# Kernel optimization log

Hardware: AMD Instinct MI355X
Metric: run time of the kernel (lower is better)

Reference implementation:

```python
import jax, jax.numpy as jnp
import numpy as np

NEG = -1000000.0

def setup_inputs() -> dict:
    key = jax.random.key(0)
    k1, k2, k3, k4 = jax.random.split(key, 4)
    B, S, D = 32, 2048, 64  # batch_eff=batch*heads, seq_len, head_dim
    queries = jax.random.normal(k1, (B, S, D), dtype=jnp.float32)
    keys = jax.random.normal(k2, (B, S, D), dtype=jnp.float32)
    values = jax.random.normal(k3, (B, S, D), dtype=jnp.float32)
    valid_len = jax.random.randint(k4, (B,), 1, S + 1, dtype=jnp.int32)
    return {"queries": queries, "keys": keys, "values": values, "valid_len": valid_len}

def reference(queries, keys, values, valid_len):
    # scores: (B, Sq, Sk) = QK^T / sqrt(d)
    d = queries.shape[-1]
    scores = jnp.einsum('bqd,bkd->bqk', queries, keys) / jnp.sqrt(jnp.float32(d))
    # padding mask from per-batch valid key lengths: True where position is padded
    k_len = keys.shape[1]
    pad_mask = jnp.arange(k_len)[None, None, :] >= valid_len[:, None, None]  # (B,1,Sk)
    scores = jnp.where(pad_mask, NEG, scores)
    attn = jax.nn.softmax(scores, axis=-1)
    # dropout is identity in eval / reference mode
    return jnp.einsum('bqk,bkd->bqd', attn, values)
```

## Files before the change

### kernel.cpp

```cpp
#include <hip/hip_runtime.h>

typedef unsigned short ushort_t;
typedef short short8 __attribute__((ext_vector_type(8)));
typedef float f32x4 __attribute__((ext_vector_type(4)));
typedef unsigned int u32x4 __attribute__((ext_vector_type(4)));

typedef f32x4 f32x4a __attribute__((may_alias));
typedef u32x4 u32x4a __attribute__((may_alias));
typedef short8 short8a __attribute__((may_alias));

#define BC 64
#define PRP 74

#define BAR_LGKM() asm volatile("s_waitcnt lgkmcnt(0)\n\ts_barrier" ::: "memory")
#define BAR_VM4()  asm volatile("s_waitcnt vmcnt(4)\n\ts_barrier" ::: "memory")
#define BAR_VM0()  asm volatile("s_waitcnt vmcnt(0)\n\ts_barrier" ::: "memory")

__device__ __forceinline__ ushort_t f2bf(float x) {
    unsigned u = __float_as_uint(x);
    u = (u + 0x7fffu + ((u >> 16) & 1u)) >> 16;
    return (ushort_t)u;
}

__device__ __forceinline__ void dma16(const void* g, void* lds) {
    __builtin_amdgcn_global_load_lds(
        (const __attribute__((address_space(1))) unsigned int*)g,
        (__attribute__((address_space(3))) unsigned int*)lds, 16, 0, 0);
}

__global__ __launch_bounds__(256) void prep_kv(
    const float* __restrict__ K, const float* __restrict__ V,
    ushort_t* __restrict__ Kb, ushort_t* __restrict__ Vt, int S, int jtiles)
{
    __shared__ ushort_t T[64 * 66];
    const int b  = blockIdx.x / jtiles;
    const int j0 = (blockIdx.x % jtiles) * 64;
    const int tid = threadIdx.x;

    {
        const int jj = tid >> 2, d0 = (tid & 3) * 16;
        const float* src = K + ((size_t)b * S + j0 + jj) * 64 + d0;
        f32x4 k0 = *(const f32x4a*)(src),     k1 = *(const f32x4a*)(src + 4);
        f32x4 k2 = *(const f32x4a*)(src + 8), k3 = *(const f32x4a*)(src + 12);
        u32x4 w0, w1;
#pragma unroll
        for (int k = 0; k < 2; ++k) {
            w0[k]   = (unsigned)f2bf(k0[2*k]) | ((unsigned)f2bf(k0[2*k+1]) << 16);
            w0[k+2] = (unsigned)f2bf(k1[2*k]) | ((unsigned)f2bf(k1[2*k+1]) << 16);
            w1[k]   = (unsigned)f2bf(k2[2*k]) | ((unsigned)f2bf(k2[2*k+1]) << 16);
            w1[k+2] = (unsigned)f2bf(k3[2*k]) | ((unsigned)f2bf(k3[2*k+1]) << 16);
        }
        ushort_t* dst = Kb + ((size_t)b * S + j0 + jj) * 64 + d0;
        *(u32x4a*)dst = w0;
        *(u32x4a*)(dst + 8) = w1;
    }

    {
        const float* Vb = V + ((size_t)b * S + j0) * 64;
#pragma unroll
        for (int p = 0; p < 4; ++p) {
            int jj = p * 16 + (tid >> 4), d4 = (tid & 15) * 4;
            f32x4 v = *(const f32x4a*)(Vb + (size_t)jj * 64 + d4);
#pragma unroll
            for (int k = 0; k < 4; ++k) T[(d4 + k) * 66 + jj] = f2bf(v[k]);
        }
        __syncthreads();
        const int d = tid >> 2, j16 = (tid & 3) * 16;
        ushort_t* dst = Vt + ((size_t)b * 64 + d) * S + j0 + j16;
        u32x4 w0, w1;
#pragma unroll
        for (int k = 0; k < 4; ++k) {
            w0[k] = (unsigned)T[d*66 + j16 + 2*k]     | ((unsigned)T[d*66 + j16 + 2*k + 1] << 16);
            w1[k] = (unsigned)T[d*66 + j16 + 8 + 2*k] | ((unsigned)T[d*66 + j16 + 9 + 2*k] << 16);
        }
        *(u32x4a*)dst = w0;
        *(u32x4a*)(dst + 8) = w1;
    }
}

__global__ __launch_bounds__(256, 3) void attn_persist(
    const float* __restrict__ Q, const ushort_t* __restrict__ Kb,
    const ushort_t* __restrict__ Vt, const int* __restrict__ VL,
    float* __restrict__ O, int* __restrict__ cnt,
    int NB, int S, int qtiles, int nitems)
{
    __shared__ __align__(16) ushort_t Kbuf[2][64 * 64];
    __shared__ __align__(16) ushort_t Vbuf[2][64 * 64];
    __shared__ ushort_t Psh[4 * 16 * PRP];
    __shared__ int order_s[64];
    __shared__ int item_s;

    const int tid  = threadIdx.x;
    const int wave = tid >> 6;
    const int lane = tid & 63;
    const int qd   = lane >> 4;
    const int c    = lane & 15;
    const int q8   = qd * 8;

    if (tid < NB && NB <= 64) {
        const int myL = VL[tid];
        int rank = 0;
        for (int j = 0; j < NB; ++j) {
            const int Lj = VL[j];
            rank += (Lj > myL) || (Lj == myL && j < tid);
        }
        order_s[rank] = tid;
    }
    __syncthreads();

    const int r0 = 8 * (wave * 2) + (lane >> 3);
    const int r1 = r0 + 8;
    const int bdp = lane & 7;
    const int swz0 = ((bdp - r0) & 7) * 16;
    const int swz1 = ((bdp - r1) & 7) * 16;
    const int ldsoff0 = (wave * 2) * 512;
    const int ldsoff1 = ldsoff0 + 512;

    int off[2][4];
#pragma unroll
    for (int x = 0; x < 2; ++x)
#pragma unroll
        for (int y = 0; y < 4; ++y) {
            const int row = y * 16 + c;
            off[x][y] = row * 128 + (((x * 4 + qd) + row) & 7) * 16;
        }

    const float qs = 0.125f * 1.4426950408889634f;
    const f32x4 zero4 = {0.0f, 0.0f, 0.0f, 0.0f};
    ushort_t* Pw = Psh + wave * (16 * PRP);

    for (;;) {
        if (tid == 0) item_s = atomicAdd(cnt, 1);
        __syncthreads();
        const int it = item_s;
        if (it >= nitems) break;

        const int b  = order_s[it / qtiles];
        const int qt = it % qtiles;
        const int qrow0 = qt * 64 + wave * 16;
        const int L   = VL[b];
        const int nkt = (L + BC - 1) / BC;

        short8 qf[2];
        {
            const float* Qb = Q + ((size_t)b * S + qrow0) * 64;
#pragma unroll
            for (int kc = 0; kc < 2; ++kc) {
                const float* p = Qb + c * 64 + kc * 32 + q8;
                f32x4 a = *(const f32x4a*)p;
                f32x4 bq = *(const f32x4a*)(p + 4);
                short8 f;
#pragma unroll
                for (int k = 0; k < 4; ++k) {
                    f[k]   = (short)f2bf(a[k] * qs);
                    f[k+4] = (short)f2bf(bq[k] * qs);
                }
                qf[kc] = f;
            }
        }

        f32x4 oacc[4];
#pragma unroll
        for (int dt = 0; dt < 4; ++dt) oacc[dt] = zero4;
        float lrow[4] = {0.0f, 0.0f, 0.0f, 0.0f};

        const char* KbB = (const char*)(Kb + (size_t)b * S * 64);
        const char* VtB = (const char*)(Vt + (size_t)b * 64 * S);
        const char* kg0 = KbB + r0 * 128 + swz0;
        const char* kg1 = KbB + r1 * 128 + swz1;
        const char* vg0 = VtB + (size_t)r0 * (S * 2) + swz0;
        const char* vg1 = VtB + (size_t)r1 * (S * 2) + swz1;

        dma16(kg0, Kbuf[0] + ldsoff0);
        dma16(kg1, Kbuf[0] + ldsoff1);
        dma16(vg0, Vbuf[0] + ldsoff0);
        dma16(vg1, Vbuf[0] + ldsoff1);

        for (int kt = 0; kt < nkt; ++kt) {
            const int j0 = kt * BC;
            const ushort_t* Kt  = Kbuf[kt & 1];
            const ushort_t* Vb_ = Vbuf[kt & 1];

            if (kt + 1 < nkt) {
                const size_t ko = (size_t)(kt + 1) * 8192;
                const size_t vo = (size_t)(kt + 1) * 128;
                ushort_t* kb = Kbuf[(kt + 1) & 1];
                ushort_t* vb = Vbuf[(kt + 1) & 1];
                dma16(kg0 + ko, kb + ldsoff0);
                dma16(kg1 + ko, kb + ldsoff1);
                dma16(vg0 + vo, vb + ldsoff0);
                dma16(vg1 + vo, vb + ldsoff1);
                BAR_VM4();
            } else {
                BAR_VM0();
            }

            f32x4 sacc[4];
#pragma unroll
            for (int nt = 0; nt < 4; ++nt) sacc[nt] = zero4;
#pragma unroll
            for (int kc = 0; kc < 2; ++kc) {
#pragma unroll
                for (int nt = 0; nt < 4; ++nt) {
                    short8 kf = *(const short8a*)((const char*)Kt + off[kc][nt]);
                    sacc[nt] = __builtin_amdgcn_mfma_f32_16x16x32_bf16(qf[kc], kf, sacc[nt], 0, 0, 0);
                }
            }

#pragma unroll
            for (int nt = 0; nt < 4; ++nt) {
                const bool valid = (j0 + nt * 16 + c) < L;
#pragma unroll
                for (int r = 0; r < 4; ++r) {
                    float p = valid ? exp2f(sacc[nt][r]) : 0.0f;
                    lrow[r] += p;
                    Pw[(qd * 4 + r) * PRP + nt * 16 + c] = f2bf(p);
                }
            }

#pragma unroll
            for (int jc = 0; jc < 2; ++jc) {
                short8 pf = *(const short8a*)&Pw[c * PRP + jc * 32 + q8];
#pragma unroll
                for (int dt = 0; dt < 4; ++dt) {
                    short8 vf = *(const short8a*)((const char*)Vb_ + off[jc][dt]);
                    oacc[dt] = __builtin_amdgcn_mfma_f32_16x16x32_bf16(pf, vf, oacc[dt], 0, 0, 0);
                }
            }

            BAR_LGKM();
        }

#pragma unroll
        for (int r = 0; r < 4; ++r) {
            float ls = lrow[r];
            ls += __shfl_xor(ls, 1);
            ls += __shfl_xor(ls, 2);
            ls += __shfl_xor(ls, 4);
            ls += __shfl_xor(ls, 8);
            const float inv = 1.0f / ls;
            const int row = qrow0 + qd * 4 + r;
            float* dst = O + ((size_t)b * S + row) * 64;
#pragma unroll
            for (int dt = 0; dt < 4; ++dt)
                dst[dt * 16 + c] = oacc[dt][r] * inv;
        }
    }
}

__global__ __launch_bounds__(256, 4) void attn_mono(
    const float* __restrict__ Q, const float* __restrict__ K,
    const float* __restrict__ V, const int* __restrict__ VL,
    float* __restrict__ O, int NB, int S)
{
    __shared__ ushort_t Ksh[BC * PRP];
    __shared__ ushort_t Vsh[64 * PRP];
    __shared__ ushort_t Psh[4 * 16 * PRP];
    const int tid = threadIdx.x, wave = tid >> 6, lane = tid & 63;
    const int qd = lane >> 4, c = lane & 15, q8 = qd * 8;
    const int bid = blockIdx.x;
    const int b = (bid & 7) | (((bid >> 3) & 3) << 3);
    const int qt = bid >> 5;
    const int qrow0 = qt * 64 + wave * 16;
    const int L = VL[b];
    const int nkt = (L + BC - 1) / BC;
    const size_t bbase = (size_t)b * S * 64;
    const int kj = tid >> 2, kd = (tid & 3) * 16;
    const int vp = tid & 31, vd = (tid >> 5) * 8;
    const float qs = 0.125f * 1.4426950408889634f;
    short8 qf[2];
    {
        const float* Qb = Q + bbase + (size_t)qrow0 * 64;
#pragma unroll
        for (int kc = 0; kc < 2; ++kc) {
            const float* p = Qb + c * 64 + kc * 32 + q8;
            f32x4 a = *(const f32x4a*)p;
            f32x4 bq = *(const f32x4a*)(p + 4);
            short8 f;
#pragma unroll
            for (int k = 0; k < 4; ++k) { f[k] = (short)f2bf(a[k]*qs); f[k+4] = (short)f2bf(bq[k]*qs); }
            qf[kc] = f;
        }
    }
    const f32x4 zero4 = {0.0f, 0.0f, 0.0f, 0.0f};
    f32x4 oacc[4];
#pragma unroll
    for (int dt = 0; dt < 4; ++dt) oacc[dt] = zero4;
    float lrow[4] = {0, 0, 0, 0};
    ushort_t* Pw = Psh + wave * (16 * PRP);
    for (int kt = 0; kt < nkt; ++kt) {
        const int j0 = kt * BC;
        __syncthreads();
        {
            const float* src = K + bbase + (size_t)(j0 + kj) * 64 + kd;
            f32x4 k0 = *(const f32x4a*)(src), k1 = *(const f32x4a*)(src + 4);
            f32x4 k2 = *(const f32x4a*)(src + 8), k3 = *(const f32x4a*)(src + 12);
            u32x4 w0, w1;
#pragma unroll
            for (int k = 0; k < 2; ++k) {
                w0[k]   = (unsigned)f2bf(k0[2*k]) | ((unsigned)f2bf(k0[2*k+1]) << 16);
                w0[k+2] = (unsigned)f2bf(k1[2*k]) | ((unsigned)f2bf(k1[2*k+1]) << 16);
                w1[k]   = (unsigned)f2bf(k2[2*k]) | ((unsigned)f2bf(k2[2*k+1]) << 16);
                w1[k+2] = (unsigned)f2bf(k3[2*k]) | ((unsigned)f2bf(k3[2*k+1]) << 16);
            }
            *(u32x4a*)&Ksh[kj * PRP + kd] = w0;
            *(u32x4a*)&Ksh[kj * PRP + kd + 8] = w1;
        }
        {
            const float* src = V + bbase + (size_t)(j0 + 2 * vp) * 64 + vd;
            f32x4 a0 = *(const f32x4a*)(src), a1 = *(const f32x4a*)(src + 4);
            f32x4 b0 = *(const f32x4a*)(src + 64), b1 = *(const f32x4a*)(src + 68);
#pragma unroll
            for (int kk = 0; kk < 8; ++kk) {
                float av = (kk < 4) ? a0[kk & 3] : a1[kk & 3];
                float bv = (kk < 4) ? b0[kk & 3] : b1[kk & 3];
                *(unsigned __attribute__((may_alias))*)&Vsh[(vd + kk) * PRP + 2 * vp] =
                    (unsigned)f2bf(av) | ((unsigned)f2bf(bv) << 16);
            }
        }
        __syncthreads();
        f32x4 sacc[4];
#pragma unroll
        for (int nt = 0; nt < 4; ++nt) sacc[nt] = zero4;
#pragma unroll
        for (int kc = 0; kc < 2; ++kc)
#pragma unroll
            for (int nt = 0; nt < 4; ++nt) {
                short8 kf = *(const short8a*)&Ksh[(nt * 16 + c) * PRP + kc * 32 + q8];
                sacc[nt] = __builtin_amdgcn_mfma_f32_16x16x32_bf16(qf[kc], kf, sacc[nt], 0, 0, 0);
            }
#pragma unroll
        for (int nt = 0; nt < 4; ++nt) {
            const bool valid = (j0 + nt * 16 + c) < L;
#pragma unroll
            for (int r = 0; r < 4; ++r) {
                float p = valid ? exp2f(sacc[nt][r]) : 0.0f;
                lrow[r] += p;
                Pw[(qd * 4 + r) * PRP + nt * 16 + c] = f2bf(p);
            }
        }
#pragma unroll
        for (int jc = 0; jc < 2; ++jc) {
            short8 pf = *(const short8a*)&Pw[c * PRP + jc * 32 + q8];
#pragma unroll
            for (int dt = 0; dt < 4; ++dt) {
                short8 vf = *(const short8a*)&Vsh[(dt * 16 + c) * PRP + jc * 32 + q8];
                oacc[dt] = __builtin_amdgcn_mfma_f32_16x16x32_bf16(pf, vf, oacc[dt], 0, 0, 0);
            }
        }
    }
#pragma unroll
    for (int r = 0; r < 4; ++r) {
        float ls = lrow[r];
        ls += __shfl_xor(ls, 1); ls += __shfl_xor(ls, 2);
        ls += __shfl_xor(ls, 4); ls += __shfl_xor(ls, 8);
        const float inv = 1.0f / ls;
        const int row = qrow0 + qd * 4 + r;
        float* dst = O + bbase + (size_t)row * 64;
#pragma unroll
        for (int dt = 0; dt < 4; ++dt) dst[dt * 16 + c] = oacc[dt][r] * inv;
    }
}

extern "C" void kernel_launch(void* const* d_in, const int* in_sizes, int n_in,
                              void* d_out, int out_size, void* d_ws, size_t ws_size,
                              hipStream_t stream) {
    const float* Q = (const float*)d_in[0];
    const float* K = (const float*)d_in[1];
    const float* V = (const float*)d_in[2];
    const int*  VL = (const int*)d_in[3];
    float*      Op = (float*)d_out;

    const int NB = in_sizes[3];
    const int S  = in_sizes[0] / (NB * 64);
    const int qtiles = S / 64;
    const int jtiles = S / 64;
    const size_t nelem = (size_t)NB * S * 64;
    const size_t bf_bytes = nelem * 2;

    if (ws_size >= 256 + 2 * bf_bytes && NB <= 64) {
        int* cnt = (int*)d_ws;
        ushort_t* Kb = (ushort_t*)((char*)d_ws + 256);
        ushort_t* Vt = (ushort_t*)((char*)d_ws + 256 + bf_bytes);
        hipMemsetAsync(d_ws, 0, 256, stream);
        prep_kv<<<dim3(NB * jtiles), dim3(256), 0, stream>>>(K, V, Kb, Vt, S, jtiles);
        const int nitems = NB * qtiles;
        attn_persist<<<dim3(768), dim3(256), 0, stream>>>(
            Q, Kb, Vt, VL, Op, cnt, NB, S, qtiles, nitems);
    } else {
        attn_mono<<<dim3(NB * qtiles), dim3(256), 0, stream>>>(Q, K, V, VL, Op, NB, S);
    }
}
```

Measured before the change: 172.7 us.

## Process two 16-row query subtiles per wave and skip padded KV tiles in prep

Each wave now handles 32 query rows instead of 16, so every K and V fragment read from LDS feeds two MFMAs and the number of work items is halved. The prep kernel exits early for key tiles beyond the valid length, avoiding conversion of padded K/V. It also switches to the hardware exp2 intrinsic. The trade-off is higher register pressure from doubled accumulators and fewer, larger work items, which gives coarser load balancing across 768 persistent blocks.

```diff
diff --git a/kernel.cpp b/kernel.cpp
--- a/kernel.cpp
+++ b/kernel.cpp
@@ -30,11 +30,14 @@
 
 __global__ __launch_bounds__(256) void prep_kv(
     const float* __restrict__ K, const float* __restrict__ V,
+    const int* __restrict__ VL,
     ushort_t* __restrict__ Kb, ushort_t* __restrict__ Vt, int S, int jtiles)
 {
     __shared__ ushort_t T[64 * 66];
     const int b  = blockIdx.x / jtiles;
-    const int j0 = (blockIdx.x % jtiles) * 64;
+    const int jt = blockIdx.x % jtiles;
+    if (jt * 64 >= VL[b]) return;
+    const int j0 = jt * 64;
     const int tid = threadIdx.x;
 
     {
@@ -82,11 +85,11 @@
     const float* __restrict__ Q, const ushort_t* __restrict__ Kb,
     const ushort_t* __restrict__ Vt, const int* __restrict__ VL,
     float* __restrict__ O, int* __restrict__ cnt,
-    int NB, int S, int qtiles, int nitems)
+    int NB, int S, int qpairs, int nitems)
 {
     __shared__ __align__(16) ushort_t Kbuf[2][64 * 64];
     __shared__ __align__(16) ushort_t Vbuf[2][64 * 64];
-    __shared__ ushort_t Psh[4 * 16 * PRP];
+    __shared__ ushort_t Psh[4 * 32 * PRP];
     __shared__ int order_s[64];
     __shared__ int item_s;
 
@@ -127,7 +130,7 @@
 
     const float qs = 0.125f * 1.4426950408889634f;
     const f32x4 zero4 = {0.0f, 0.0f, 0.0f, 0.0f};
-    ushort_t* Pw = Psh + wave * (16 * PRP);
+    ushort_t* Pw = Psh + wave * (32 * PRP);
 
     for (;;) {
         if (tid == 0) item_s = atomicAdd(cnt, 1);
@@ -135,34 +138,38 @@
         const int it = item_s;
         if (it >= nitems) break;
 
-        const int b  = order_s[it / qtiles];
-        const int qt = it % qtiles;
-        const int qrow0 = qt * 64 + wave * 16;
+        const int b  = order_s[it / qpairs];
+        const int qp = it % qpairs;
+        const int qrow0 = qp * 128 + wave * 32;
         const int L   = VL[b];
         const int nkt = (L + BC - 1) / BC;
 
-        short8 qf[2];
+        short8 qf[2][2];
         {
             const float* Qb = Q + ((size_t)b * S + qrow0) * 64;
 #pragma unroll
-            for (int kc = 0; kc < 2; ++kc) {
-                const float* p = Qb + c * 64 + kc * 32 + q8;
-                f32x4 a = *(const f32x4a*)p;
-                f32x4 bq = *(const f32x4a*)(p + 4);
-                short8 f;
-#pragma unroll
-                for (int k = 0; k < 4; ++k) {
-                    f[k]   = (short)f2bf(a[k] * qs);
-                    f[k+4] = (short)f2bf(bq[k] * qs);
+            for (int sub = 0; sub < 2; ++sub)
+#pragma unroll
+                for (int kc = 0; kc < 2; ++kc) {
+                    const float* p = Qb + (sub * 16 + c) * 64 + kc * 32 + q8;
+                    f32x4 a = *(const f32x4a*)p;
+                    f32x4 bq = *(const f32x4a*)(p + 4);
+                    short8 f;
+#pragma unroll
+                    for (int k = 0; k < 4; ++k) {
+                        f[k]   = (short)f2bf(a[k] * qs);
+                        f[k+4] = (short)f2bf(bq[k] * qs);
+                    }
+                    qf[sub][kc] = f;
                 }
-                qf[kc] = f;
-            }
-        }
-
-        f32x4 oacc[4];
-#pragma unroll
-        for (int dt = 0; dt < 4; ++dt) oacc[dt] = zero4;
-        float lrow[4] = {0.0f, 0.0f, 0.0f, 0.0f};
+        }
+
+        f32x4 oacc[2][4];
+#pragma unroll
+        for (int sub = 0; sub < 2; ++sub)
+#pragma unroll
+            for (int dt = 0; dt < 4; ++dt) oacc[sub][dt] = zero4;
+        float lrow[2][4] = {{0,0,0,0},{0,0,0,0}};
 
         const char* KbB = (const char*)(Kb + (size_t)b * S * 64);
         const char* VtB = (const char*)(Vt + (size_t)b * 64 * S);
@@ -195,15 +202,18 @@
                 BAR_VM0();
             }
 
-            f32x4 sacc[4];
-#pragma unroll
-            for (int nt = 0; nt < 4; ++nt) sacc[nt] = zero4;
+            f32x4 sacc[2][4];
+#pragma unroll
+            for (int sub = 0; sub < 2; ++sub)
+#pragma unroll
+                for (int nt = 0; nt < 4; ++nt) sacc[sub][nt] = zero4;
 #pragma unroll
             for (int kc = 0; kc < 2; ++kc) {
 #pragma unroll
                 for (int nt = 0; nt < 4; ++nt) {
                     short8 kf = *(const short8a*)((const char*)Kt + off[kc][nt]);
-                    sacc[nt] = __builtin_amdgcn_mfma_f32_16x16x32_bf16(qf[kc], kf, sacc[nt], 0, 0, 0);
+                    sacc[0][nt] = __builtin_amdgcn_mfma_f32_16x16x32_bf16(qf[0][kc], kf, sacc[0][nt], 0, 0, 0);
+                    sacc[1][nt] = __builtin_amdgcn_mfma_f32_16x16x32_bf16(qf[1][kc], kf, sacc[1][nt], 0, 0, 0);
                 }
             }
 
@@ -211,20 +221,24 @@
             for (int nt = 0; nt < 4; ++nt) {
                 const bool valid = (j0 + nt * 16 + c) < L;
 #pragma unroll
-                for (int r = 0; r < 4; ++r) {
-                    float p = valid ? exp2f(sacc[nt][r]) : 0.0f;
-                    lrow[r] += p;
-                    Pw[(qd * 4 + r) * PRP + nt * 16 + c] = f2bf(p);
-                }
+                for (int sub = 0; sub < 2; ++sub)
+#pragma unroll
+                    for (int r = 0; r < 4; ++r) {
+                        float p = valid ? __builtin_amdgcn_exp2f(sacc[sub][nt][r]) : 0.0f;
+                        lrow[sub][r] += p;
+                        Pw[(sub * 16 + qd * 4 + r) * PRP + nt * 16 + c] = f2bf(p);
+                    }
             }
 
 #pragma unroll
             for (int jc = 0; jc < 2; ++jc) {
-                short8 pf = *(const short8a*)&Pw[c * PRP + jc * 32 + q8];
+                short8 pf0 = *(const short8a*)&Pw[(0 * 16 + c) * PRP + jc * 32 + q8];
+                short8 pf1 = *(const short8a*)&Pw[(1 * 16 + c) * PRP + jc * 32 + q8];
 #pragma unroll
                 for (int dt = 0; dt < 4; ++dt) {
                     short8 vf = *(const short8a*)((const char*)Vb_ + off[jc][dt]);
-                    oacc[dt] = __builtin_amdgcn_mfma_f32_16x16x32_bf16(pf, vf, oacc[dt], 0, 0, 0);
+                    oacc[0][dt] = __builtin_amdgcn_mfma_f32_16x16x32_bf16(pf0, vf, oacc[0][dt], 0, 0, 0);
+                    oacc[1][dt] = __builtin_amdgcn_mfma_f32_16x16x32_bf16(pf1, vf, oacc[1][dt], 0, 0, 0);
                 }
             }
 
@@ -232,19 +246,21 @@
         }
 
 #pragma unroll
-        for (int r = 0; r < 4; ++r) {
-            float ls = lrow[r];
-            ls += __shfl_xor(ls, 1);
-            ls += __shfl_xor(ls, 2);
-            ls += __shfl_xor(ls, 4);
-            ls += __shfl_xor(ls, 8);
-            const float inv = 1.0f / ls;
-            const int row = qrow0 + qd * 4 + r;
-            float* dst = O + ((size_t)b * S + row) * 64;
-#pragma unroll
-            for (int dt = 0; dt < 4; ++dt)
-                dst[dt * 16 + c] = oacc[dt][r] * inv;
-        }
+        for (int sub = 0; sub < 2; ++sub)
+#pragma unroll
+            for (int r = 0; r < 4; ++r) {
+                float ls = lrow[sub][r];
+                ls += __shfl_xor(ls, 1);
+                ls += __shfl_xor(ls, 2);
+                ls += __shfl_xor(ls, 4);
+                ls += __shfl_xor(ls, 8);
+                const float inv = 1.0f / ls;
+                const int row = qrow0 + sub * 16 + qd * 4 + r;
+                float* dst = O + ((size_t)b * S + row) * 64;
+#pragma unroll
+                for (int dt = 0; dt < 4; ++dt)
+                    dst[dt * 16 + c] = oacc[sub][dt][r] * inv;
+            }
     }
 }
 
@@ -259,8 +275,8 @@
     const int tid = threadIdx.x, wave = tid >> 6, lane = tid & 63;
     const int qd = lane >> 4, c = lane & 15, q8 = qd * 8;
     const int bid = blockIdx.x;
-    const int b = (bid & 7) | (((bid >> 3) & 3) << 3);
-    const int qt = bid >> 5;
+    const int b = bid % NB;
+    const int qt = bid / NB;
     const int qrow0 = qt * 64 + wave * 16;
     const int L = VL[b];
     const int nkt = (L + BC - 1) / BC;
@@ -334,7 +350,7 @@
             const bool valid = (j0 + nt * 16 + c) < L;
 #pragma unroll
             for (int r = 0; r < 4; ++r) {
-                float p = valid ? exp2f(sacc[nt][r]) : 0.0f;
+                float p = valid ? __builtin_amdgcn_exp2f(sacc[nt][r]) : 0.0f;
                 lrow[r] += p;
                 Pw[(qd * 4 + r) * PRP + nt * 16 + c] = f2bf(p);
             }
@@ -373,21 +389,21 @@
 
     const int NB = in_sizes[3];
     const int S  = in_sizes[0] / (NB * 64);
-    const int qtiles = S / 64;
     const int jtiles = S / 64;
     const size_t nelem = (size_t)NB * S * 64;
     const size_t bf_bytes = nelem * 2;
 
-    if (ws_size >= 256 + 2 * bf_bytes && NB <= 64) {
+    if (ws_size >= 256 + 2 * bf_bytes && NB <= 64 && (S % 128) == 0) {
         int* cnt = (int*)d_ws;
         ushort_t* Kb = (ushort_t*)((char*)d_ws + 256);
         ushort_t* Vt = (ushort_t*)((char*)d_ws + 256 + bf_bytes);
         hipMemsetAsync(d_ws, 0, 256, stream);
-        prep_kv<<<dim3(NB * jtiles), dim3(256), 0, stream>>>(K, V, Kb, Vt, S, jtiles);
-        const int nitems = NB * qtiles;
+        prep_kv<<<dim3(NB * jtiles), dim3(256), 0, stream>>>(K, V, VL, Kb, Vt, S, jtiles);
+        const int qpairs = S / 128;
+        const int nitems = NB * qpairs;
         attn_persist<<<dim3(768), dim3(256), 0, stream>>>(
-            Q, Kb, Vt, VL, Op, cnt, NB, S, qtiles, nitems);
+            Q, Kb, Vt, VL, Op, cnt, NB, S, qpairs, nitems);
     } else {
-        attn_mono<<<dim3(NB * qtiles), dim3(256), 0, stream>>>(Q, K, V, VL, Op, NB, S);
-    }
-}
+        attn_mono<<<dim3(NB * (S / 64)), dim3(256), 0, stream>>>(Q, K, V, VL, Op, NB, S);
+    }
+}
```

Result: slower. 208.1 us (+20.5%).
